# Kernel tuning notes

Hardware: AMD Instinct MI355X
Metric: run time of the kernel (lower is better)

Reference implementation:

```python
import jax, jax.numpy as jnp
import numpy as np

B, D_IN, H1, H2, D_OUT = 1024, 2048, 4096, 4096, 1024

def setup_inputs() -> dict:
    key = jax.random.key(0)
    ks = jax.random.split(key, 8)
    scale = lambda fan_in: 1.0 / np.sqrt(fan_in)
    x  = jax.random.normal(ks[0], (B, D_IN), dtype=jnp.float32)
    W1 = jax.random.normal(ks[1], (H1, D_IN), dtype=jnp.float32) * scale(D_IN)
    b1 = jax.random.normal(ks[2], (H1,), dtype=jnp.float32) * scale(D_IN)
    W2 = jax.random.normal(ks[3], (H2, H1), dtype=jnp.float32) * scale(H1)
    b2 = jax.random.normal(ks[4], (H2,), dtype=jnp.float32) * scale(H1)
    W3 = jax.random.normal(ks[5], (D_OUT, H2), dtype=jnp.float32) * scale(H2)
    b3 = jax.random.normal(ks[6], (D_OUT,), dtype=jnp.float32) * scale(H2)
    b_taus = jnp.array([2.0, 1.0, 0.5], dtype=jnp.float32)
    return {"x": x, "W1": W1, "b1": b1, "W2": W2, "b2": b2, "W3": W3, "b3": b3, "b_taus": b_taus, "T": 10}

def reference(x, W1, b1, W2, b2, W3, b3, b_taus, T):
    # x: [B, D_IN] (already flat). betas are scalar sigmoid gates, constant over time.
    beta1, beta2, beta3 = jax.nn.sigmoid(b_taus)
    s1 = jnp.zeros((x.shape[0], W1.shape[0]), dtype=x.dtype)
    s2 = jnp.zeros((x.shape[0], W2.shape[0]), dtype=x.dtype)
    s3 = jnp.zeros((x.shape[0], W3.shape[0]), dtype=x.dtype)

    def step(carry, _):
        s1, s2, s3 = carry
        d1 = jax.nn.relu(x @ W1.T + b1)
        s1 = beta1 * s1 + (1 - beta1) * d1
        d2 = jax.nn.relu(s1 @ W2.T + b2)
        s2 = beta2 * s2 + (1 - beta2) * d2
        d3 = s2 @ W3.T + b3
        s3 = beta3 * s3 + (1 - beta3) * d3
        return (s1, s2, s3), None

    (s1, s2, s3), _ = jax.lax.scan(step, (s1, s2, s3), None, length=T)
    return s3
```

## Files before the change

kernel.cpp:

```cpp
#include <hip/hip_runtime.h>
#include <hip/hip_bf16.h>
#include <stdint.h>

#define AS_GLOBAL __attribute__((address_space(1)))
#define AS_LDS    __attribute__((address_space(3)))

typedef __attribute__((ext_vector_type(8))) short  bf16x8;
typedef __attribute__((ext_vector_type(4))) float  f32x4;
typedef __attribute__((ext_vector_type(8))) short  s16x8;

__device__ __forceinline__ void gload_lds16(const void* g, void* l) {
    __builtin_amdgcn_global_load_lds((AS_GLOBAL const void*)g, (AS_LDS void*)l, 16, 0, 0);
}

__device__ __forceinline__ void cast_pair(const float* __restrict__ s,
                                          __hip_bfloat16* __restrict__ d, long p) {
    f32x4 a = ((const f32x4*)s)[p * 2];
    f32x4 b = ((const f32x4*)s)[p * 2 + 1];
    union { s16x8 p8; __hip_bfloat16 h[8]; } u;
    u.h[0] = __float2bfloat16(a.x); u.h[1] = __float2bfloat16(a.y);
    u.h[2] = __float2bfloat16(a.z); u.h[3] = __float2bfloat16(a.w);
    u.h[4] = __float2bfloat16(b.x); u.h[5] = __float2bfloat16(b.y);
    u.h[6] = __float2bfloat16(b.z); u.h[7] = __float2bfloat16(b.w);
    ((s16x8*)d)[p] = u.p8;
}

__global__ void cast_all_k(const float* __restrict__ x,  __hip_bfloat16* __restrict__ xb,
                           const float* __restrict__ W1, __hip_bfloat16* __restrict__ W1b,
                           const float* __restrict__ W2, __hip_bfloat16* __restrict__ W2b,
                           const float* __restrict__ W3, __hip_bfloat16* __restrict__ W3b) {
    const long n0 = 262144, n1 = n0 + 1048576, n2 = n1 + 2097152, n3 = n2 + 524288;
    const long stride = 2048L * 256;
    for (long p = (long)blockIdx.x * 256 + threadIdx.x; p < n3; p += stride) {
        if      (p < n0) cast_pair(x,  xb,  p);
        else if (p < n1) cast_pair(W1, W1b, p - n0);
        else if (p < n2) cast_pair(W2, W2b, p - n1);
        else             cast_pair(W3, W3b, p - n2);
    }
}

template <int TAG>
__global__ __launch_bounds__(256, 4)
void gemm_l(const __hip_bfloat16* __restrict__ A,
            const __hip_bfloat16* __restrict__ Bm,
            __hip_bfloat16* __restrict__ P,
            const int M, const int N, const int kchunk, const int S)
{
    __shared__ __hip_bfloat16 As[128 * 64];
    __shared__ __hip_bfloat16 Bs[128 * 64];

    const int tid = threadIdx.x;
    const int bn = blockIdx.x, bm = blockIdx.y, kz = blockIdx.z;

    const int lane = tid & 63;
    const int wave = tid >> 6;
    const int wm   = wave >> 1, wn = wave & 1;
    const int lm   = lane & 15, lq = lane >> 4;

    const int K  = kchunk * S;
    const int k0 = kz * kchunk;

    const int rlo  = lane >> 3;
    const int gsw8 = (((lane & 7) ^ rlo) << 3);

    const __hip_bfloat16* Ag = A  + (size_t)(bm * 128) * K;
    const __hip_bfloat16* Bg = Bm + (size_t)(bn * 128) * K;

    f32x4 acc[4][4];
    #pragma unroll
    for (int i = 0; i < 4; ++i)
        #pragma unroll
        for (int j = 0; j < 4; ++j)
            acc[i][j] = (f32x4){0.f, 0.f, 0.f, 0.f};

    for (int kt = k0; kt < k0 + kchunk; kt += 64) {
        __syncthreads();
        #pragma unroll
        for (int c = 0; c < 4; ++c) {
            const int chunk = wave * 4 + c;
            const int row   = chunk * 8 + rlo;
            gload_lds16(Ag + (size_t)row * K + kt + gsw8, As + chunk * 512);
            gload_lds16(Bg + (size_t)row * K + kt + gsw8, Bs + chunk * 512);
        }
        __syncthreads();
        #pragma unroll
        for (int kk = 0; kk < 2; ++kk) {
            const int sl = (((kk * 4 + lq) ^ (lm & 7)) << 3);
            bf16x8 af[4], bq[4];
            #pragma unroll
            for (int i = 0; i < 4; ++i)
                af[i] = *(const bf16x8*)(As + (wm * 64 + i * 16 + lm) * 64 + sl);
            #pragma unroll
            for (int j = 0; j < 4; ++j)
                bq[j] = *(const bf16x8*)(Bs + (wn * 64 + j * 16 + lm) * 64 + sl);
            #pragma unroll
            for (int i = 0; i < 4; ++i)
                #pragma unroll
                for (int j = 0; j < 4; ++j)
                    acc[i][j] = __builtin_amdgcn_mfma_f32_16x16x32_bf16(af[i], bq[j], acc[i][j], 0, 0, 0);
        }
    }

    __hip_bfloat16* Pz = P + (size_t)kz * M * N;
    const int row0 = bm * 128 + wm * 64;
    const int colb = bn * 128 + wn * 64 + lm;
    #pragma unroll
    for (int j = 0; j < 4; ++j) {
        const int col = colb + j * 16;
        #pragma unroll
        for (int i = 0; i < 4; ++i)
            #pragma unroll
            for (int r = 0; r < 4; ++r) {
                const int row = row0 + i * 16 + lq * 4 + r;
                Pz[(size_t)row * N + col] = __float2bfloat16(acc[i][j][r]);
            }
    }
}

template <int TT>
__device__ __forceinline__ void tcollapse_coef(float be1, float be2, float be3,
                                               float* __restrict__ c, float* __restrict__ w) {
    float g[TT + 1];
    g[TT] = 1.f;
    float p3 = 1.f;
    #pragma unroll
    for (int u = TT - 1; u >= 1; --u) {
        p3 *= be3;
        g[u] = be2 * g[u + 1] + p3;
    }
    const float s = (1.f - be2) * (1.f - be3);
    float p1 = 1.f;
    #pragma unroll
    for (int u = 1; u <= TT; ++u) {
        p1 *= be1;
        c[u - 1] = 1.f - p1;
        w[u - 1] = s * g[u];
    }
}

template <int MODE>
__global__ void reduce_k(const __hip_bfloat16* __restrict__ P, const int S,
                         void* __restrict__ outv, const long MN, const int N,
                         const float* __restrict__ bias,
                         const float* __restrict__ b_taus,
                         const int* __restrict__ Tp)
{
    long i8 = (long)blockIdx.x * 256 + threadIdx.x;
    long i  = i8 * 8;
    float a[8] = {0.f, 0.f, 0.f, 0.f, 0.f, 0.f, 0.f, 0.f};
    for (int s = 0; s < S; ++s) {
        union { s16x8 p8; __hip_bfloat16 h[8]; } u;
        u.p8 = *(const s16x8*)(P + (size_t)s * MN + i);
        #pragma unroll
        for (int c = 0; c < 8; ++c) a[c] += __bfloat162float(u.h[c]);
    }
    const int col = (int)(i % N);
    float bb[8];
    #pragma unroll
    for (int c = 0; c < 8; ++c) bb[c] = bias[col + c];

    if constexpr (MODE == 0) {
        union { s16x8 p8; __hip_bfloat16 h[8]; } u;
        #pragma unroll
        for (int c = 0; c < 8; ++c)
            u.h[c] = __float2bfloat16(fmaxf(a[c] + bb[c], 0.f));
        ((s16x8*)outv)[i8] = u.p8;
    } else if constexpr (MODE == 1) {
        const int   T   = *Tp;
        const float be1 = 1.f / (1.f + expf(-b_taus[0]));
        const float be2 = 1.f / (1.f + expf(-b_taus[1]));
        const float be3 = 1.f / (1.f + expf(-b_taus[2]));
        union { s16x8 p8; __hip_bfloat16 h[8]; } u;
        if (T == 10) {
            float c10[10], w10[10];
            tcollapse_coef<10>(be1, be2, be3, c10, w10);
            #pragma unroll
            for (int c = 0; c < 8; ++c) {
                float za = 0.f;
                #pragma unroll
                for (int t = 0; t < 10; ++t)
                    za += w10[t] * fmaxf(fmaf(c10[t], a[c], bb[c]), 0.f);
                u.h[c] = __float2bfloat16(za);
            }
        } else {
            #pragma unroll
            for (int c = 0; c < 8; ++c) {
                float p1 = 1.f, s2 = 0.f, za = 0.f;
                for (int t = 0; t < T; ++t) {
                    p1 *= be1;
                    const float d2 = fmaxf(fmaf(1.f - p1, a[c], bb[c]), 0.f);
                    s2 = be2 * s2 + (1.f - be2) * d2;
                    za = be3 * za + (1.f - be3) * s2;
                }
                u.h[c] = __float2bfloat16(za);
            }
        }
        ((s16x8*)outv)[i8] = u.p8;
    } else {
        const int   T   = *Tp;
        const float be3 = 1.f / (1.f + expf(-b_taus[2]));
        float g = 0.f;
        for (int t = 0; t < T; ++t) g = be3 * g + (1.f - be3);
        f32x4 o0, o1;
        o0.x = a[0] + g * bb[0]; o0.y = a[1] + g * bb[1];
        o0.z = a[2] + g * bb[2]; o0.w = a[3] + g * bb[3];
        o1.x = a[4] + g * bb[4]; o1.y = a[5] + g * bb[5];
        o1.z = a[6] + g * bb[6]; o1.w = a[7] + g * bb[7];
        ((f32x4*)outv)[i8 * 2]     = o0;
        ((f32x4*)outv)[i8 * 2 + 1] = o1;
    }
}

extern "C" void kernel_launch(void* const* d_in, const int* in_sizes, int n_in,
                              void* d_out, int out_size, void* d_ws, size_t ws_size,
                              hipStream_t stream) {
    const float* x      = (const float*)d_in[0];
    const float* W1     = (const float*)d_in[1];
    const float* b1     = (const float*)d_in[2];
    const float* W2     = (const float*)d_in[3];
    const float* b2     = (const float*)d_in[4];
    const float* W3     = (const float*)d_in[5];
    const float* b3     = (const float*)d_in[6];
    const float* b_taus = (const float*)d_in[7];
    const int*   Tp     = (const int*)d_in[8];

    const int B = 1024, DIN = 2048, H1 = 4096, H2 = 4096, DOUT = 1024;
    const long MB = 1024 * 1024;

    char* ws = (char*)d_ws;
    __hip_bfloat16* xb  = (__hip_bfloat16*)(ws + 0);
    __hip_bfloat16* W1b = (__hip_bfloat16*)(ws + 4 * MB);
    __hip_bfloat16* W2b = (__hip_bfloat16*)(ws + 20 * MB);
    __hip_bfloat16* W3b = (__hip_bfloat16*)(ws + 52 * MB);
    __hip_bfloat16* D1b = (__hip_bfloat16*)(ws + 60 * MB);
    __hip_bfloat16* Sb  = (__hip_bfloat16*)(ws + 68 * MB);
    __hip_bfloat16* Pb  = (__hip_bfloat16*)(ws + 76 * MB);

    cast_all_k<<<dim3(2048), dim3(256), 0, stream>>>(x, xb, W1, W1b, W2, W2b, W3, W3b);

    gemm_l<1><<<dim3(H1 / 128, B / 128, 2), 256, 0, stream>>>(
        xb, W1b, Pb, B, H1, DIN / 2, 2);
    reduce_k<0><<<dim3(2048), 256, 0, stream>>>(Pb, 2, (void*)D1b, (long)B * H1, H1, b1, nullptr, nullptr);

    gemm_l<2><<<dim3(H2 / 128, B / 128, 4), 256, 0, stream>>>(
        D1b, W2b, Pb, B, H2, H1 / 4, 4);
    reduce_k<1><<<dim3(2048), 256, 0, stream>>>(Pb, 4, (void*)Sb, (long)B * H2, H2, b2, b_taus, Tp);

    gemm_l<3><<<dim3(DOUT / 128, B / 128, 8), 256, 0, stream>>>(
        Sb, W3b, Pb, B, DOUT, H2 / 8, 8);
    reduce_k<2><<<dim3(512), 256, 0, stream>>>(Pb, 8, d_out, (long)B * DOUT, DOUT, b3, b_taus, Tp);
}
```

Measured before the change: 260.9 us.

## Fuse fp32-to-bf16 weight conversion into GEMM tile loads

Drops the standalone kernel that casts all weights to bf16 and instead loads fp32 weight tiles straight into LDS, converting to bf16 when fragments are read for MFMA. This removes a full extra read and write pass over about 28M weight elements. In exchange the B tile doubles in LDS size, occupancy is lowered to 3 blocks, B-side global traffic per GEMM doubles, and each weight element is reconverted by every block row that reads it.

```diff
diff --git a/kernel.cpp b/kernel.cpp
--- a/kernel.cpp
+++ b/kernel.cpp
@@ -25,29 +25,20 @@
     ((s16x8*)d)[p] = u.p8;
 }
 
-__global__ void cast_all_k(const float* __restrict__ x,  __hip_bfloat16* __restrict__ xb,
-                           const float* __restrict__ W1, __hip_bfloat16* __restrict__ W1b,
-                           const float* __restrict__ W2, __hip_bfloat16* __restrict__ W2b,
-                           const float* __restrict__ W3, __hip_bfloat16* __restrict__ W3b) {
-    const long n0 = 262144, n1 = n0 + 1048576, n2 = n1 + 2097152, n3 = n2 + 524288;
-    const long stride = 2048L * 256;
-    for (long p = (long)blockIdx.x * 256 + threadIdx.x; p < n3; p += stride) {
-        if      (p < n0) cast_pair(x,  xb,  p);
-        else if (p < n1) cast_pair(W1, W1b, p - n0);
-        else if (p < n2) cast_pair(W2, W2b, p - n1);
-        else             cast_pair(W3, W3b, p - n2);
-    }
+__global__ void cast_x_k(const float* __restrict__ x, __hip_bfloat16* __restrict__ xb) {
+    long p = (long)blockIdx.x * 256 + threadIdx.x;
+    cast_pair(x, xb, p);
 }
 
 template <int TAG>
-__global__ __launch_bounds__(256, 4)
-void gemm_l(const __hip_bfloat16* __restrict__ A,
-            const __hip_bfloat16* __restrict__ Bm,
+__global__ __launch_bounds__(256, 3)
+void gemm_f(const __hip_bfloat16* __restrict__ A,
+            const float* __restrict__ Bf,
             __hip_bfloat16* __restrict__ P,
             const int M, const int N, const int kchunk, const int S)
 {
     __shared__ __hip_bfloat16 As[128 * 64];
-    __shared__ __hip_bfloat16 Bs[128 * 64];
+    __shared__ float          BsF[128 * 64];
 
     const int tid = threadIdx.x;
     const int bn = blockIdx.x, bm = blockIdx.y, kz = blockIdx.z;
@@ -60,11 +51,15 @@
     const int K  = kchunk * S;
     const int k0 = kz * kchunk;
 
-    const int rlo  = lane >> 3;
-    const int gsw8 = (((lane & 7) ^ rlo) << 3);
+    const int rloA = lane >> 3;
+    const int gswA = (((lane & 7) ^ rloA) << 3);
+
+    const int rloB = lane >> 4;
+    const int hB   = (lane >> 3) & 1;
+    const int s7B  = lane & 7;
 
     const __hip_bfloat16* Ag = A  + (size_t)(bm * 128) * K;
-    const __hip_bfloat16* Bg = Bm + (size_t)(bn * 128) * K;
+    const float*          Bg = Bf + (size_t)(bn * 128) * K;
 
     f32x4 acc[4][4];
     #pragma unroll
@@ -78,21 +73,37 @@
         #pragma unroll
         for (int c = 0; c < 4; ++c) {
             const int chunk = wave * 4 + c;
-            const int row   = chunk * 8 + rlo;
-            gload_lds16(Ag + (size_t)row * K + kt + gsw8, As + chunk * 512);
-            gload_lds16(Bg + (size_t)row * K + kt + gsw8, Bs + chunk * 512);
+            const int row   = chunk * 8 + rloA;
+            gload_lds16(Ag + (size_t)row * K + kt + gswA, As + chunk * 512);
+        }
+        #pragma unroll
+        for (int c = 0; c < 8; ++c) {
+            const int q   = wave * 8 + c;
+            const int row = q * 4 + rloB;
+            const int f7  = s7B ^ (row & 7);
+            gload_lds16(Bg + (size_t)row * K + kt + f7 * 8 + hB * 4, BsF + q * 256);
         }
         __syncthreads();
         #pragma unroll
         for (int kk = 0; kk < 2; ++kk) {
-            const int sl = (((kk * 4 + lq) ^ (lm & 7)) << 3);
+            const int slA = (((kk * 4 + lq) ^ (lm & 7)) << 3);
+            const int fB  = (kk * 4 + lq) ^ (lm & 7);
             bf16x8 af[4], bq[4];
             #pragma unroll
             for (int i = 0; i < 4; ++i)
-                af[i] = *(const bf16x8*)(As + (wm * 64 + i * 16 + lm) * 64 + sl);
-            #pragma unroll
-            for (int j = 0; j < 4; ++j)
-                bq[j] = *(const bf16x8*)(Bs + (wn * 64 + j * 16 + lm) * 64 + sl);
+                af[i] = *(const bf16x8*)(As + (wm * 64 + i * 16 + lm) * 64 + slA);
+            #pragma unroll
+            for (int j = 0; j < 4; ++j) {
+                const float* bp = BsF + (wn * 64 + j * 16 + lm) * 64;
+                f32x4 b0 = *(const f32x4*)(bp + fB * 4);
+                f32x4 b1 = *(const f32x4*)(bp + 32 + fB * 4);
+                union { s16x8 p8; __hip_bfloat16 h[8]; } u;
+                u.h[0] = __float2bfloat16(b0.x); u.h[1] = __float2bfloat16(b0.y);
+                u.h[2] = __float2bfloat16(b0.z); u.h[3] = __float2bfloat16(b0.w);
+                u.h[4] = __float2bfloat16(b1.x); u.h[5] = __float2bfloat16(b1.y);
+                u.h[6] = __float2bfloat16(b1.z); u.h[7] = __float2bfloat16(b1.w);
+                bq[j] = (bf16x8)u.p8;
+            }
             #pragma unroll
             for (int i = 0; i < 4; ++i)
                 #pragma unroll
@@ -229,24 +240,21 @@
 
     char* ws = (char*)d_ws;
     __hip_bfloat16* xb  = (__hip_bfloat16*)(ws + 0);
-    __hip_bfloat16* W1b = (__hip_bfloat16*)(ws + 4 * MB);
-    __hip_bfloat16* W2b = (__hip_bfloat16*)(ws + 20 * MB);
-    __hip_bfloat16* W3b = (__hip_bfloat16*)(ws + 52 * MB);
-    __hip_bfloat16* D1b = (__hip_bfloat16*)(ws + 60 * MB);
-    __hip_bfloat16* Sb  = (__hip_bfloat16*)(ws + 68 * MB);
-    __hip_bfloat16* Pb  = (__hip_bfloat16*)(ws + 76 * MB);
-
-    cast_all_k<<<dim3(2048), dim3(256), 0, stream>>>(x, xb, W1, W1b, W2, W2b, W3, W3b);
-
-    gemm_l<1><<<dim3(H1 / 128, B / 128, 2), 256, 0, stream>>>(
-        xb, W1b, Pb, B, H1, DIN / 2, 2);
+    __hip_bfloat16* D1b = (__hip_bfloat16*)(ws + 4 * MB);
+    __hip_bfloat16* Sb  = (__hip_bfloat16*)(ws + 12 * MB);
+    __hip_bfloat16* Pb  = (__hip_bfloat16*)(ws + 20 * MB);
+
+    cast_x_k<<<dim3(1024), dim3(256), 0, stream>>>(x, xb);
+
+    gemm_f<1><<<dim3(H1 / 128, B / 128, 2), 256, 0, stream>>>(
+        xb, W1, Pb, B, H1, DIN / 2, 2);
     reduce_k<0><<<dim3(2048), 256, 0, stream>>>(Pb, 2, (void*)D1b, (long)B * H1, H1, b1, nullptr, nullptr);
 
-    gemm_l<2><<<dim3(H2 / 128, B / 128, 4), 256, 0, stream>>>(
-        D1b, W2b, Pb, B, H2, H1 / 4, 4);
+    gemm_f<2><<<dim3(H2 / 128, B / 128, 4), 256, 0, stream>>>(
+        D1b, W2, Pb, B, H2, H1 / 4, 4);
     reduce_k<1><<<dim3(2048), 256, 0, stream>>>(Pb, 4, (void*)Sb, (long)B * H2, H2, b2, b_taus, Tp);
 
-    gemm_l<3><<<dim3(DOUT / 128, B / 128, 8), 256, 0, stream>>>(
-        Sb, W3b, Pb, B, DOUT, H2 / 8, 8);
+    gemm_f<3><<<dim3(DOUT / 128, B / 128, 8), 256, 0, stream>>>(
+        Sb, W3, Pb, B, DOUT, H2 / 8, 8);
     reduce_k<2><<<dim3(512), 256, 0, stream>>>(Pb, 8, d_out, (long)B * DOUT, DOUT, b3, b_taus, Tp);
 }
```

New measurement: 277.4 us. +6.3%, slower.
